# Optimization experiments

Measured on AMD Instinct MI355X. Metric: run time of the kernel, lower is better.

Reference implementation:

```python
import jax, jax.numpy as jnp
import numpy as np

D_MODEL = 2048; D_STATE = 128; D_CONV = 4; EXPAND = 2
HEADDIM = 64; NGROUPS = 1; CHUNK = 256
D_INNER = EXPAND * D_MODEL          # 4096
NHEADS = D_INNER // HEADDIM         # 64
HG = NHEADS // NGROUPS              # heads per group
CONV_DIM = D_INNER + 2 * NGROUPS * D_STATE          # 4352
D_IN_PROJ = 2 * D_INNER + 2 * NGROUPS * D_STATE + NHEADS  # 8512
BATCH = 2; SEQLEN = 2048
EPS = 1e-5


def setup_inputs() -> dict:
    ks = jax.random.split(jax.random.key(0), 8)
    u = jax.random.normal(ks[0], (BATCH, SEQLEN, D_MODEL), jnp.float32)
    in_proj_w = jax.random.normal(ks[1], (D_IN_PROJ, D_MODEL), jnp.float32) * D_MODEL ** -0.5
    conv_w = jax.random.normal(ks[2], (CONV_DIM, D_CONV), jnp.float32) * D_CONV ** -0.5
    conv_b = jax.random.normal(ks[3], (CONV_DIM,), jnp.float32) * 0.1
    # dt_bias init exactly as in the module: inv softplus of dt ~ U(log(1e-3), log(1e-1))
    dt = jnp.exp(jax.random.uniform(ks[4], (NHEADS,), jnp.float32)
                 * (np.float32(np.log(0.1)) - np.float32(np.log(0.001))) + np.float32(np.log(0.001)))
    dt = jnp.clip(dt, 1e-4, None)
    dt_bias = dt + jnp.log(-jnp.expm1(-dt))
    A_log = jnp.log(jax.random.uniform(ks[5], (NHEADS,), jnp.float32, minval=1.0, maxval=16.0))
    D_skip = jnp.ones((NHEADS,), jnp.float32)
    norm_w = jnp.ones((D_INNER,), jnp.float32)
    out_proj_w = jax.random.normal(ks[6], (D_MODEL, D_INNER), jnp.float32) * D_INNER ** -0.5
    return dict(u=u, in_proj_w=in_proj_w, conv_w=conv_w, conv_b=conv_b,
                dt_bias=dt_bias, A_log=A_log, D_skip=D_skip,
                norm_w=norm_w, out_proj_w=out_proj_w)


def _mamba2(u, in_proj_w, conv_w, conv_b, dt_bias, A_log, D_skip, norm_w, out_proj_w):
    b, l, _ = u.shape
    nc = l // CHUNK
    zxbcdt = u @ in_proj_w.T                                   # (b,l,d_in_proj)
    z = zxbcdt[..., :D_INNER]                                  # gate
    xBC = zxbcdt[..., D_INNER:D_INNER + CONV_DIM]
    dt = jax.nn.softplus(zxbcdt[..., D_INNER + CONV_DIM:] + dt_bias)  # (b,l,h)
    # causal depthwise conv1d (padding d_conv-1, truncated to seqlen) + SiLU
    xp = jnp.pad(xBC, ((0, 0), (D_CONV - 1, 0), (0, 0)))
    conv = conv_b + sum(conv_w[:, k] * xp[:, k:k + l, :] for k in range(D_CONV))
    xBC = jax.nn.silu(conv)
    x = xBC[..., :D_INNER].reshape(b, l, NHEADS, HEADDIM)
    Bm = xBC[..., D_INNER:D_INNER + NGROUPS * D_STATE].reshape(b, l, NGROUPS, D_STATE)
    Cm = xBC[..., D_INNER + NGROUPS * D_STATE:].reshape(b, l, NGROUPS, D_STATE)
    A = -jnp.exp(A_log)                                        # (h,)
    # ---- SSD chunked scan ----
    xc = x.reshape(b, nc, CHUNK, NGROUPS, HG, HEADDIM)         # (b,c,s,g,H,p)
    dtc = dt.reshape(b, nc, CHUNK, NGROUPS, HG)                # (b,c,s,g,H)
    Bc = Bm.reshape(b, nc, CHUNK, NGROUPS, D_STATE)            # (b,c,s,g,n)
    Cc = Cm.reshape(b, nc, CHUNK, NGROUPS, D_STATE)
    dA = jnp.transpose(dtc * A.reshape(NGROUPS, HG), (0, 3, 4, 1, 2))  # (b,g,H,c,s)
    dA_cs = jnp.cumsum(dA, axis=-1)                            # (b,g,H,c,s)
    # intra-chunk: L[i,j] = exp(sum_{j<k<=i} dA_k), lower-triangular (diag=1)
    seg = dA_cs[..., :, None] - dA_cs[..., None, :]            # (b,g,H,c,l,s)
    tri = jnp.tril(jnp.ones((CHUNK, CHUNK), bool))
    Lmat = jnp.where(tri, jnp.exp(seg), 0.0)
    xdt = xc * dtc[..., None]                                  # (b,c,s,g,H,p)
    CB = jnp.einsum('bclgn,bcsgn->bcgls', Cc, Bc)
    Y_diag = jnp.einsum('bcgls,bgHcls,bcsgHp->bclgHp', CB, Lmat, xdt)
    # chunk states and inter-chunk recurrence
    decay_states = jnp.exp(dA_cs[..., -1:] - dA_cs)            # (b,g,H,c,s)
    states = jnp.einsum('bcsgn,bgHcs,bcsgHp->bcgHpn', Bc, decay_states, xdt)
    chunk_decay = jnp.exp(dA_cs[..., -1])                      # (b,g,H,c)

    def step(carry, inp):
        st, dec = inp
        return carry * dec[..., None, None] + st, carry

    _, prev = jax.lax.scan(step, jnp.zeros_like(states[:, 0]),
                           (jnp.moveaxis(states, 1, 0), jnp.moveaxis(chunk_decay, -1, 0)))
    prev = jnp.moveaxis(prev, 0, 1)                            # (b,c,g,H,p,n) state entering chunk
    Y_off = jnp.einsum('bclgn,bcgHpn,bgHcl->bclgHp', Cc, prev, jnp.exp(dA_cs))
    y = (Y_diag + Y_off).reshape(b, l, NHEADS, HEADDIM) + x * D_skip[None, None, :, None]
    y = y.reshape(b, l, D_INNER)
    # gated RMSNorm: gate first (norm_before_gate=False), groupwise rms (ngroups=1 -> full)
    y = y * jax.nn.silu(z)
    yg = y.reshape(b, l, NGROUPS, D_INNER // NGROUPS)
    yg = yg * jax.lax.rsqrt(jnp.mean(yg * yg, axis=-1, keepdims=True) + EPS)
    y = yg.reshape(b, l, D_INNER) * norm_w
    return y @ out_proj_w.T                                    # (b,l,d_model)


def reference(u, in_proj_w, conv_w, conv_b, dt_bias, A_log, D_skip, norm_w, out_proj_w):
    return _mamba2(u, in_proj_w, conv_w, conv_b, dt_bias, A_log, D_skip, norm_w, out_proj_w)
```

## Files before the change

### kernel.cpp

```cpp
#include <hip/hip_runtime.h>
#include <hip/hip_bf16.h>


#define D_MODEL   2048
#define D_STATE   128
#define HEADDIM   64
#define CHUNK     256
#define D_INNER   4096
#define NHEADS    64
#define CONV_DIM  4352
#define D_IN_PROJ 8512
#define SEQLEN    2048
#define NC        8
#define ROWSTOT   4096
#define NPAD      8576
#define RMS_EPS   1e-5f

#define OFF_WIN   0ull
#define OFF_XBF   0ull
#define OFF_PREV  0ull
#define OFF_WOUT  16777216ull
#define OFF_UBF   35127296ull
#define OFF_DTV   35127296ull
#define OFF_DACS  36175872ull
#define OFF_BBF   37224448ull
#define OFF_CBF   38273024ull
#define OFF_CB    39321600ull
#define OFF_BT    43515904ull
#define OFF_XBC   51904512ull
#define OFF_STATE 51904512ull
#define OFF_ZBF   87556096ull
#define OFF_DTRAW 121110528ull
#define OFF_YBUF  121110528ull
#define WS_NEEDED 154664960ull

#define N4_U    2097152l
#define N4_WIN  4390912l

typedef __hip_bfloat16 bf16;
typedef __bf16 bfrag8 __attribute__((ext_vector_type(8)));
typedef float  f32x4v __attribute__((ext_vector_type(4)));

__device__ __forceinline__ f32x4v mfma16(bfrag8 a, bfrag8 b, f32x4v c) {
  return __builtin_amdgcn_mfma_f32_16x16x32_bf16(a, b, c, 0, 0, 0);
}

__device__ __forceinline__ void gload_lds16(const void* g, void* l) {
  __builtin_amdgcn_global_load_lds((const __attribute__((address_space(1))) void*)g,
                                   (__attribute__((address_space(3))) void*)l, 16, 0, 0);
}

__device__ __forceinline__ bf16 f2b(float x) { return __float2bfloat16(x); }
__device__ __forceinline__ float b2f(bf16 x) { return __bfloat162float(x); }
__device__ __forceinline__ float siluf(float x) { return x / (1.f + __expf(-x)); }

#define BARRIER() asm volatile("s_barrier" ::: "memory")
#define WAITV(N) asm volatile("s_waitcnt vmcnt(" #N ")" ::: "memory")
#define LGKM0()  asm volatile("s_waitcnt lgkmcnt(0)" ::: "memory")

__device__ __forceinline__ bfrag8 ds_read_b128f(const bf16* p) {
  bfrag8 d;
  unsigned a = (unsigned)(unsigned long long)p;
  asm volatile("ds_read_b128 %0, %1" : "=&v"(d) : "v"(a));
  return d;
}

__global__ __launch_bounds__(256) void cast_all_kernel(const float* __restrict__ u,
    const float* __restrict__ w_in,
    bf16* __restrict__ u_bf, bf16* __restrict__ win_bf) {
  long i = (long)blockIdx.x * 256 + threadIdx.x;
  if (i < N4_U) {
    float4 v = ((const float4*)u)[i];
    bf16* o = u_bf + i * 4;
    o[0] = f2b(v.x); o[1] = f2b(v.y); o[2] = f2b(v.z); o[3] = f2b(v.w);
  } else if (i < N4_U + N4_WIN) {
    long e = (i - N4_U) * 4;
    long row = e / D_MODEL;
    bf16* o = win_bf + e;
    if (row < D_IN_PROJ) {
      float4 v = *(const float4*)(w_in + e);
      o[0] = f2b(v.x); o[1] = f2b(v.y); o[2] = f2b(v.z); o[3] = f2b(v.w);
    } else {
      bf16 z = f2b(0.f);
      o[0] = z; o[1] = z; o[2] = z; o[3] = z;
    }
  }
}


__global__ __launch_bounds__(512) void gemm1_kernel(const bf16* __restrict__ A,
                                                    const bf16* __restrict__ B,
                                                    bf16* __restrict__ zb,
                                                    bf16* __restrict__ xbc,
                                                    float* __restrict__ dtraw) {
  int pid = blockIdx.x;
  int t = pid & 63, s = pid >> 6;
  int sm = s / 9, sn = s % 9;
  int xcd = t & 7, j8 = t >> 3;
  int tm = sm * 8 + (xcd >> 1) * 2 + (j8 & 1);
  int tn = sn * 8 + (xcd & 1) * 4 + (j8 >> 1);
  if (tn >= 67) return;
  long row0 = (long)tm * 256, col0 = (long)tn * 128;

  __shared__ __align__(16) bf16 As[2 * 256 * 32];
  __shared__ __align__(16) bf16 Bs[2 * 128 * 32];
  int tid = threadIdx.x, lane = tid & 63, w = tid >> 6;
  int wr = w >> 1, wc = w & 1, r16 = lane & 15, q = lane >> 4;
  int qs = (q ^ ((r16 >> 1) & 3)) * 8;
  const int K = D_MODEL;
  f32x4v zero4 = {0.f, 0.f, 0.f, 0.f};
  f32x4v acc[4][4];
#pragma unroll
  for (int i = 0; i < 4; ++i)
#pragma unroll
    for (int j = 0; j < 4; ++j) acc[i][j] = zero4;

  for (int kt = 0; kt < K; kt += 64) {
    __syncthreads();
#pragma unroll
    for (int j = 0; j < 4; ++j) {
      int ci = j * 512 + tid;
      int half = ci >> 10, cj = ci & 1023;
      int r = cj >> 2;
      int ko = half * 32 + ((cj & 3) ^ ((cj >> 3) & 3)) * 8;
      gload_lds16(A + (row0 + r) * (long)K + kt + ko,
                  (char*)As + j * 8192 + w * 1024);
    }
#pragma unroll
    for (int j = 0; j < 2; ++j) {
      int ci = j * 512 + tid;
      int half = ci >> 9, cj = ci & 511;
      int r = cj >> 2;
      int ko = half * 32 + ((cj & 3) ^ ((cj >> 3) & 3)) * 8;
      gload_lds16(B + (col0 + r) * (long)K + kt + ko,
                  (char*)Bs + j * 8192 + w * 1024);
    }
    __syncthreads();
#pragma unroll
    for (int ks = 0; ks < 2; ++ks) {
      const bf16* Ab = As + ks * 8192;
      const bf16* Bb = Bs + ks * 4096;
      bfrag8 af[4], bfv[4];
#pragma unroll
      for (int i = 0; i < 4; ++i) af[i]  = *(const bfrag8*)(Ab + (wr * 64 + i * 16 + r16) * 32 + qs);
#pragma unroll
      for (int i = 0; i < 4; ++i) bfv[i] = *(const bfrag8*)(Bb + (wc * 64 + i * 16 + r16) * 32 + qs);
#pragma unroll
      for (int i = 0; i < 4; ++i)
#pragma unroll
        for (int j = 0; j < 4; ++j) acc[i][j] = mfma16(af[i], bfv[j], acc[i][j]);
    }
  }
#pragma unroll
  for (int i = 0; i < 4; ++i)
#pragma unroll
    for (int j = 0; j < 4; ++j) {
      long col = col0 + wc * 64 + j * 16 + r16;
#pragma unroll
      for (int r = 0; r < 4; ++r) {
        long row = row0 + wr * 64 + i * 16 + q * 4 + r;
        float v = acc[i][j][r];
        if (col < D_INNER)                       zb[row * D_INNER + col] = f2b(v);
        else if (col < D_INNER + CONV_DIM)       xbc[row * CONV_DIM + (col - D_INNER)] = f2b(v);
        else if (col < D_IN_PROJ)                dtraw[row * NHEADS + (col - D_INNER - CONV_DIM)] = v;
      }
    }
}

template<int LD>
__device__ __forceinline__ void stage_half2(const bf16* __restrict__ src,
    long rowbeg, int kt, char* lds_slot, int tid, int w) {
  int r = tid >> 2;
  int ko0 = ((tid & 3) ^ ((tid >> 3) & 3)) * 8;
  const bf16* g0 = src + (rowbeg + r) * (long)LD + kt + ko0;
  gload_lds16(g0,      lds_slot + w * 1024);
  gload_lds16(g0 + 32, lds_slot + 8192 + w * 1024);
}

__global__ __launch_bounds__(512, 2) void gemm2_kernel(const bf16* __restrict__ A,
                                                       const bf16* __restrict__ Bw,
                                                       float* __restrict__ C) {
  int pid = blockIdx.x;
  int tn = (pid & 7) * 2 + (pid >> 7);
  int tm = (pid >> 3) & 15;
  long row0 = (long)tm * 256, col0 = (long)tn * 128;

  __shared__ __align__(16) bf16 As[6 * 8192];
  __shared__ __align__(16) bf16 Bs[3 * 8192];
  char* AsB = (char*)&As[0];
  char* BsB = (char*)&Bs[0];

  int tid = threadIdx.x, lane = tid & 63, w = tid >> 6;
  int r16 = lane & 15, qh = lane >> 4;
  int qs = (qh ^ ((r16 >> 1) & 3)) * 8;
  int wm = w >> 1, wn = w & 1;
  int hsel = wm >> 1;
  int rih = (wm & 1) * 64 + r16;
  int cb = wn * 64 + r16;

  f32x4v zero4 = {0.f, 0.f, 0.f, 0.f};
  f32x4v acc[4][4];
#pragma unroll
  for (int i = 0; i < 4; ++i)
#pragma unroll
    for (int j = 0; j < 4; ++j) acc[i][j] = zero4;

  stage_half2<D_INNER>(A,  row0,       0,  AsB + 0 * 16384, tid, w);
  stage_half2<D_INNER>(Bw, col0,       0,  BsB + 0 * 16384, tid, w);
  stage_half2<D_INNER>(A,  row0 + 128, 0,  AsB + 1 * 16384, tid, w);
  stage_half2<D_INNER>(A,  row0,       64, AsB + 2 * 16384, tid, w);
  stage_half2<D_INNER>(Bw, col0,       64, BsB + 1 * 16384, tid, w);
  stage_half2<D_INNER>(A,  row0 + 128, 64, AsB + 3 * 16384, tid, w);
  WAITV(6);
  BARRIER();

  int cur = 0, pf = 2;
#pragma unroll 1
  for (int tt = 0; tt < 64; ++tt) {
    int kpref = (tt < 62 ? tt + 2 : 63) * 64;
    const bf16* Asl = As + (cur * 2 + hsel) * 8192;
    const bf16* Bsl = Bs + cur * 8192;
    bfrag8 af[4], bfv[4];

#pragma unroll
    for (int i = 0; i < 4; ++i) af[i]  = ds_read_b128f(Asl + (rih + i * 16) * 32 + qs);
#pragma unroll
    for (int j = 0; j < 4; ++j) bfv[j] = ds_read_b128f(Bsl + (cb + j * 16) * 32 + qs);
    stage_half2<D_INNER>(A,  row0,       kpref, AsB + (pf * 2) * 16384, tid, w);
    stage_half2<D_INNER>(Bw, col0,       kpref, BsB + pf * 16384, tid, w);
    BARRIER();
    LGKM0();
    __builtin_amdgcn_sched_barrier(0);
    __builtin_amdgcn_s_setprio(1);
#pragma unroll
    for (int i = 0; i < 4; ++i)
#pragma unroll
      for (int j = 0; j < 4; ++j) acc[i][j] = mfma16(af[i], bfv[j], acc[i][j]);
    __builtin_amdgcn_s_setprio(0);
    BARRIER();

#pragma unroll
    for (int i = 0; i < 4; ++i) af[i]  = ds_read_b128f(Asl + 4096 + (rih + i * 16) * 32 + qs);
#pragma unroll
    for (int j = 0; j < 4; ++j) bfv[j] = ds_read_b128f(Bsl + 4096 + (cb + j * 16) * 32 + qs);
    stage_half2<D_INNER>(A,  row0 + 128, kpref, AsB + (pf * 2 + 1) * 16384, tid, w);
    WAITV(6);
    BARRIER();
    LGKM0();
    __builtin_amdgcn_sched_barrier(0);
    __builtin_amdgcn_s_setprio(1);
#pragma unroll
    for (int i = 0; i < 4; ++i)
#pragma unroll
      for (int j = 0; j < 4; ++j) acc[i][j] = mfma16(af[i], bfv[j], acc[i][j]);
    __builtin_amdgcn_s_setprio(0);
    BARRIER();

    cur = (cur == 2) ? 0 : cur + 1;
    pf  = (pf  == 2) ? 0 : pf + 1;
  }
  WAITV(0);

#pragma unroll
  for (int i = 0; i < 4; ++i)
#pragma unroll
    for (int j = 0; j < 4; ++j)
#pragma unroll
      for (int r = 0; r < 4; ++r) {
        long row = row0 + wm * 64 + i * 16 + qh * 4 + r;
        long col = col0 + wn * 64 + j * 16 + r16;
        C[row * (long)D_MODEL + col] = acc[i][j][r];
      }
}

__global__ __launch_bounds__(256) void conv_dt_kernel(
    const float* __restrict__ dtraw, const float* __restrict__ dt_bias,
    const float* __restrict__ A_log, float* __restrict__ dtv_buf,
    float* __restrict__ dacs_buf,
    const bf16* __restrict__ xbc, const float* __restrict__ conv_w,
    const float* __restrict__ conv_b, bf16* __restrict__ xo,
    bf16* __restrict__ Bo, bf16* __restrict__ Co, bf16* __restrict__ BT) {
  if (blockIdx.x < 1024) {
    int blk = blockIdx.x;
    int c = blk & 7, h = (blk >> 3) & 63, b = blk >> 9;
    int s = threadIdx.x, lane = s & 63, w = s >> 6;
    long row = (long)b * SEQLEN + c * CHUNK + s;
    float raw = dtraw[row * NHEADS + h] + dt_bias[h];
    float dtv = fmaxf(raw, 0.f) + log1pf(__expf(-fabsf(raw)));
    float A = -__expf(A_log[h]);
    float x = dtv * A;
#pragma unroll
    for (int off = 1; off < 64; off <<= 1) {
      float y = __shfl_up(x, off);
      if (lane >= off) x += y;
    }
    __shared__ __align__(16) float wsum[4];
    if (lane == 63) wsum[w] = x;
    __syncthreads();
    float pre = 0.f;
#pragma unroll
    for (int i = 0; i < 4; ++i) pre += (i < w) ? wsum[i] : 0.f;
    long o = ((long)(b * NHEADS + h) * NC + c) * CHUNK + s;
    dtv_buf[o] = dtv;
    dacs_buf[o] = x + pre;
    return;
  }
  int t = blockIdx.x - 1024;
  int bx = t % 17;
  int rest = t / 17;
  int by = rest & 255, bz = rest >> 8;
  int cidx = bx * 256 + threadIdx.x;
  int l0 = by * 8, b = bz;
  float4 wv = *(const float4*)(conv_w + cidx * 4);
  float bias = conv_b[cidx];
  const bf16* base = xbc + (long)b * SEQLEN * CONV_DIM + cidx;
  float win[11];
#pragma unroll
  for (int k = 0; k < 11; ++k) {
    int ls = l0 - 3 + k;
    win[k] = (ls >= 0) ? b2f(base[(long)ls * CONV_DIM]) : 0.f;
  }
  int cgrp = (cidx < D_INNER) ? 0 : ((cidx < D_INNER + D_STATE) ? 1 : 2);
  int n = cidx - D_INNER;
  int n2 = cidx - D_INNER - D_STATE;
  int cch = l0 >> 8;
#pragma unroll
  for (int j = 0; j < 8; ++j) {
    float acc = bias + wv.x * win[j] + wv.y * win[j + 1] + wv.z * win[j + 2] + wv.w * win[j + 3];
    bf16 o = f2b(siluf(acc));
    int l = l0 + j;
    long rowo = (long)b * SEQLEN + l;
    if (cgrp == 0) {
      xo[rowo * D_INNER + cidx] = o;
    } else if (cgrp == 1) {
      Bo[rowo * D_STATE + n] = o;
      BT[(((long)b * NC + cch) * D_STATE + n) * CHUNK + (l & 255)] = o;
    } else {
      Co[rowo * D_STATE + n2] = o;
    }
  }
}

__global__ __launch_bounds__(256) void cb_kernel(const bf16* __restrict__ Cg,
                                                 const bf16* __restrict__ Bg,
                                                 float* __restrict__ CB) {
  int blk = blockIdx.x;
  int stile = blk & 3, bc = blk >> 2;
  int c = bc & 7, b = bc >> 3;
  int tid = threadIdx.x, lane = tid & 63, w = tid >> 6, r16 = lane & 15, q = lane >> 4;
  const bf16* Cb = Cg + ((long)b * SEQLEN + c * CHUNK) * D_STATE;
  const bf16* Bb = Bg + ((long)b * SEQLEN + c * CHUNK) * D_STATE;
  bfrag8 af[4][4];
#pragma unroll
  for (int lt = 0; lt < 4; ++lt)
#pragma unroll
    for (int kk = 0; kk < 4; ++kk)
      af[lt][kk] = *(const bfrag8*)(Cb + (long)(w * 64 + lt * 16 + r16) * D_STATE + kk * 32 + q * 8);
  float* CBb = CB + (long)bc * CHUNK * CHUNK;
  f32x4v zero4 = {0.f, 0.f, 0.f, 0.f};
  for (int st = stile * 4; st < stile * 4 + 4; ++st) {
    f32x4v acc[4] = {zero4, zero4, zero4, zero4};
#pragma unroll
    for (int kk = 0; kk < 4; ++kk) {
      bfrag8 bfv = *(const bfrag8*)(Bb + (long)(st * 16 + r16) * D_STATE + kk * 32 + q * 8);
#pragma unroll
      for (int lt = 0; lt < 4; ++lt) acc[lt] = mfma16(af[lt][kk], bfv, acc[lt]);
    }
#pragma unroll
    for (int lt = 0; lt < 4; ++lt)
#pragma unroll
      for (int r = 0; r < 4; ++r)
        CBb[(long)(w * 64 + lt * 16 + q * 4 + r) * CHUNK + st * 16 + r16] = acc[lt][r];
  }
}

__global__ __launch_bounds__(256) void ssm_diag_kernel(
    const bf16* __restrict__ xg, const bf16* __restrict__ BT,
    const float* __restrict__ CB, const float* __restrict__ dtv_buf,
    const float* __restrict__ dacs_buf, const float* __restrict__ Dskip,
    bf16* __restrict__ ybuf, float* __restrict__ states) {
  int blk = blockIdx.x;
  int h = blk & 63, cc = (blk >> 6) & 7, b = blk >> 9;
  int tid = threadIdx.x, lane = tid & 63, w = tid >> 6, r16 = lane & 15, q = lane >> 4;

  __shared__ __align__(16) __bf16 xT[HEADDIM][264];
  __shared__ __align__(16) float cs_s[CHUNK];
  __shared__ __align__(16) float dt_s[CHUNK];
  __shared__ __align__(16) float w_s[CHUNK];

  long hco = ((long)(b * NHEADS + h) * NC + cc) * CHUNK;
  cs_s[tid] = dacs_buf[hco + tid];
  dt_s[tid] = dtv_buf[hco + tid];
  __syncthreads();
  float cl_last = cs_s[CHUNK - 1];
  w_s[tid] = __expf(cl_last - cs_s[tid]) * dt_s[tid];

  const __bf16* xbase = (const __bf16*)(xg + ((long)b * SEQLEN + cc * CHUNK) * D_INNER + h * HEADDIM);
#pragma unroll
  for (int it = 0; it < 8; ++it) {
    int e = it * 256 + tid;
    int s = e >> 3, p0 = (e & 7) * 8;
    bfrag8 xv = *(const bfrag8*)(xbase + (long)s * D_INNER + p0);
#pragma unroll
    for (int j = 0; j < 8; ++j) xT[p0 + j][s] = xv[j];
  }
  __syncthreads();

  const float* CBchunk = CB + (long)(b * NC + cc) * CHUNK * CHUNK;
  const __bf16* BTc = (const __bf16*)(BT + (((long)b * NC + cc) * D_STATE) * CHUNK);
  f32x4v zero4 = {0.f, 0.f, 0.f, 0.f};
  f32x4v accY[4][4], accS[2][4];
#pragma unroll
  for (int i = 0; i < 4; ++i)
#pragma unroll
    for (int j = 0; j < 4; ++j) accY[i][j] = zero4;
#pragma unroll
  for (int i = 0; i < 2; ++i)
#pragma unroll
    for (int j = 0; j < 4; ++j) accS[i][j] = zero4;

  int l_row[4];
  const float* CBrow[4];
#pragma unroll
  for (int lt = 0; lt < 4; ++lt) {
    l_row[lt] = w * 64 + lt * 16 + r16;
    CBrow[lt] = CBchunk + (long)l_row[lt] * CHUNK;
  }

#pragma unroll 2
  for (int ks = 0; ks < 8; ++ks) {
    int s0 = ks * 32 + q * 8;
    float4 cs0 = *(const float4*)(cs_s + s0);
    float4 cs1 = *(const float4*)(cs_s + s0 + 4);
    float4 dt0 = *(const float4*)(dt_s + s0);
    float4 dt1 = *(const float4*)(dt_s + s0 + 4);
    float4 w0  = *(const float4*)(w_s + s0);
    float4 w1  = *(const float4*)(w_s + s0 + 4);
    float csv[8] = {cs0.x, cs0.y, cs0.z, cs0.w, cs1.x, cs1.y, cs1.z, cs1.w};
    float dtv8[8] = {dt0.x, dt0.y, dt0.z, dt0.w, dt1.x, dt1.y, dt1.z, dt1.w};
    float wv8[8]  = {w0.x, w0.y, w0.z, w0.w, w1.x, w1.y, w1.z, w1.w};

    bfrag8 xf[4];
#pragma unroll
    for (int pt = 0; pt < 4; ++pt) xf[pt] = *(const bfrag8*)(&xT[pt * 16 + r16][s0]);

#pragma unroll
    for (int lt = 0; lt < 4; ++lt) {
      int l = l_row[lt];
      float cs_l = cs_s[l];
      float4 cb0 = *(const float4*)(CBrow[lt] + s0);
      float4 cb1 = *(const float4*)(CBrow[lt] + s0 + 4);
      float cbv[8] = {cb0.x, cb0.y, cb0.z, cb0.w, cb1.x, cb1.y, cb1.z, cb1.w};
      bfrag8 pf;
#pragma unroll
      for (int j = 0; j < 8; ++j) {
        float v = (s0 + j <= l)
                    ? cbv[j] * __expf(fminf(cs_l - csv[j], 0.f)) * dtv8[j]
                    : 0.f;
        pf[j] = (__bf16)v;
      }
#pragma unroll
      for (int pt = 0; pt < 4; ++pt) accY[lt][pt] = mfma16(pf, xf[pt], accY[lt][pt]);
    }

#pragma unroll
    for (int nt = 0; nt < 2; ++nt) {
      int n = w * 32 + nt * 16 + r16;
      bfrag8 braw = *(const bfrag8*)(BTc + (long)n * CHUNK + s0);
      bfrag8 bwf;
#pragma unroll
      for (int j = 0; j < 8; ++j) bwf[j] = (__bf16)((float)braw[j] * wv8[j]);
#pragma unroll
      for (int pt = 0; pt < 4; ++pt) accS[nt][pt] = mfma16(bwf, xf[pt], accS[nt][pt]);
    }
  }

  float dsk = Dskip[h];
  bf16* ybase = ybuf + ((long)b * SEQLEN + cc * CHUNK) * D_INNER + h * HEADDIM;
#pragma unroll
  for (int lt = 0; lt < 4; ++lt)
#pragma unroll
    for (int pt = 0; pt < 4; ++pt)
#pragma unroll
      for (int r = 0; r < 4; ++r) {
        int lrow = w * 64 + lt * 16 + q * 4 + r;
        int pcol = pt * 16 + r16;
        ybase[(long)lrow * D_INNER + pcol] = f2b(accY[lt][pt][r] + (float)xT[pcol][lrow] * dsk);
      }
  float* sbase = states + (long)blk * (HEADDIM * D_STATE);
#pragma unroll
  for (int nt = 0; nt < 2; ++nt)
#pragma unroll
    for (int pt = 0; pt < 4; ++pt)
#pragma unroll
      for (int r = 0; r < 4; ++r)
        sbase[(long)(pt * 16 + r16) * D_STATE + w * 32 + nt * 16 + q * 4 + r] = accS[nt][pt][r];
}

__global__ __launch_bounds__(256) void state_scan_kernel(const float* __restrict__ states,
    const float* __restrict__ dacs, bf16* __restrict__ prevb) {
  int gid = blockIdx.x;
  int et = gid & 31, bh = gid >> 5;
  int h = bh & 63, b = bh >> 6;
  int e = et * 256 + threadIdx.x;
  float dec[NC];
#pragma unroll
  for (int c = 0; c < NC; ++c)
    dec[c] = __expf(dacs[((long)(b * NHEADS + h) * NC + c) * CHUNK + (CHUNK - 1)]);
  float carry = 0.f;
#pragma unroll
  for (int c = 0; c < NC; ++c) {
    long off = ((long)((b * NC + c) * NHEADS + h)) * (HEADDIM * D_STATE) + e;
    prevb[off] = f2b(carry);
    carry = carry * dec[c] + states[off];
  }
}

__global__ __launch_bounds__(256) void yoff_kernel(const bf16* __restrict__ Cg,
    const bf16* __restrict__ prevb, const float* __restrict__ dacs,
    bf16* __restrict__ ybuf) {
  int blk = blockIdx.x;
  int h = blk & 63, cc = (blk >> 6) & 7, b = blk >> 9;
  int tid = threadIdx.x, lane = tid & 63, w = tid >> 6, r16 = lane & 15, q = lane >> 4;
  __shared__ __align__(16) float cs_s[CHUNK];
  cs_s[tid] = dacs[((long)(b * NHEADS + h) * NC + cc) * CHUNK + tid];
  __syncthreads();
  const bf16* Cb = Cg + ((long)b * SEQLEN + cc * CHUNK) * D_STATE;
  const bf16* Pb = prevb + (long)blk * (HEADDIM * D_STATE);
  f32x4v zero4 = {0.f, 0.f, 0.f, 0.f};
  f32x4v acc[4][4];
#pragma unroll
  for (int i = 0; i < 4; ++i)
#pragma unroll
    for (int j = 0; j < 4; ++j) acc[i][j] = zero4;
#pragma unroll
  for (int kk = 0; kk < 4; ++kk) {
    bfrag8 bv[4];
#pragma unroll
    for (int pt = 0; pt < 4; ++pt)
      bv[pt] = *(const bfrag8*)(Pb + (long)(pt * 16 + r16) * D_STATE + kk * 32 + q * 8);
#pragma unroll
    for (int lt = 0; lt < 4; ++lt) {
      bfrag8 av = *(const bfrag8*)(Cb + (long)(w * 64 + lt * 16 + r16) * D_STATE + kk * 32 + q * 8);
#pragma unroll
      for (int pt = 0; pt < 4; ++pt) acc[lt][pt] = mfma16(av, bv[pt], acc[lt][pt]);
    }
  }
  bf16* ybase = ybuf + ((long)b * SEQLEN + cc * CHUNK) * D_INNER + h * HEADDIM;
#pragma unroll
  for (int lt = 0; lt < 4; ++lt)
#pragma unroll
    for (int pt = 0; pt < 4; ++pt)
#pragma unroll
      for (int r = 0; r < 4; ++r) {
        int lrow = w * 64 + lt * 16 + q * 4 + r;
        float ef = __expf(cs_s[lrow]);
        bf16* p = ybase + (long)lrow * D_INNER + pt * 16 + r16;
        *p = f2b(b2f(*p) + acc[lt][pt][r] * ef);
      }
}

__global__ __launch_bounds__(256) void cast_gate_kernel(
    const float* __restrict__ w_out, bf16* __restrict__ wout_bf,
    bf16* __restrict__ ybuf, const bf16* __restrict__ zb,
    const float* __restrict__ norm_w) {
  if (blockIdx.x < 8192) {
    long i = (long)blockIdx.x * 256 + threadIdx.x;
    float4 v = ((const float4*)w_out)[i];
    bf16* o = wout_bf + i * 4;
    o[0] = f2b(v.x); o[1] = f2b(v.y); o[2] = f2b(v.z); o[3] = f2b(v.w);
    return;
  }
  int row = blockIdx.x - 8192, tid = threadIdx.x;
  bf16* y = ybuf + (long)row * D_INNER;
  const bf16* z = zb + (long)row * D_INNER;
  float v[16];
  float ss = 0.f;
#pragma unroll
  for (int i = 0; i < 2; ++i) {
    int e = tid * 16 + i * 8;
    bfrag8 yv = *(const bfrag8*)(y + e);
    bfrag8 zv = *(const bfrag8*)(z + e);
#pragma unroll
    for (int j = 0; j < 8; ++j) {
      float a = (float)yv[j] * siluf((float)zv[j]);
      v[i * 8 + j] = a;
      ss += a * a;
    }
  }
#pragma unroll
  for (int off = 32; off > 0; off >>= 1) ss += __shfl_down(ss, off);
  __shared__ __align__(16) float red[4];
  int lane = tid & 63, w = tid >> 6;
  if (lane == 0) red[w] = ss;
  __syncthreads();
  float tot = red[0] + red[1] + red[2] + red[3];
  float scale = rsqrtf(tot * (1.f / D_INNER) + RMS_EPS);
#pragma unroll
  for (int i = 0; i < 2; ++i) {
    int e = tid * 16 + i * 8;
    float4 w0 = *(const float4*)(norm_w + e);
    float4 w1 = *(const float4*)(norm_w + e + 4);
    bfrag8 o;
    o[0] = (__bf16)(v[i * 8 + 0] * scale * w0.x);
    o[1] = (__bf16)(v[i * 8 + 1] * scale * w0.y);
    o[2] = (__bf16)(v[i * 8 + 2] * scale * w0.z);
    o[3] = (__bf16)(v[i * 8 + 3] * scale * w0.w);
    o[4] = (__bf16)(v[i * 8 + 4] * scale * w1.x);
    o[5] = (__bf16)(v[i * 8 + 5] * scale * w1.y);
    o[6] = (__bf16)(v[i * 8 + 6] * scale * w1.z);
    o[7] = (__bf16)(v[i * 8 + 7] * scale * w1.w);
    *(bfrag8*)(y + e) = o;
  }
}

extern "C" void kernel_launch(void* const* d_in, const int* in_sizes, int n_in,
                              void* d_out, int out_size, void* d_ws, size_t ws_size,
                              hipStream_t stream) {
  if (ws_size < WS_NEEDED) return;

  const float* u       = (const float*)d_in[0];
  const float* w_in    = (const float*)d_in[1];
  const float* conv_w  = (const float*)d_in[2];
  const float* conv_b  = (const float*)d_in[3];
  const float* dt_bias = (const float*)d_in[4];
  const float* A_log   = (const float*)d_in[5];
  const float* Dskip   = (const float*)d_in[6];
  const float* norm_w  = (const float*)d_in[7];
  const float* w_out   = (const float*)d_in[8];
  float* out = (float*)d_out;

  char* ws = (char*)d_ws;
  bf16*  win_bf  = (bf16*)(ws + OFF_WIN);
  bf16*  x_bf    = (bf16*)(ws + OFF_XBF);
  bf16*  prevb   = (bf16*)(ws + OFF_PREV);
  bf16*  wout_bf = (bf16*)(ws + OFF_WOUT);
  bf16*  u_bf    = (bf16*)(ws + OFF_UBF);
  float* dtv     = (float*)(ws + OFF_DTV);
  float* dacs    = (float*)(ws + OFF_DACS);
  bf16*  B_bf    = (bf16*)(ws + OFF_BBF);
  bf16*  C_bf    = (bf16*)(ws + OFF_CBF);
  float* CBb     = (float*)(ws + OFF_CB);
  bf16*  BT_bf   = (bf16*)(ws + OFF_BT);
  bf16*  xbc_bf  = (bf16*)(ws + OFF_XBC);
  float* states  = (float*)(ws + OFF_STATE);
  bf16*  z_bf    = (bf16*)(ws + OFF_ZBF);
  float* dt_raw  = (float*)(ws + OFF_DTRAW);
  bf16*  ybuf    = (bf16*)(ws + OFF_YBUF);

  cast_all_kernel<<<25344, 256, 0, stream>>>(u, w_in, u_bf, win_bf);
  gemm1_kernel<<<1152, 512, 0, stream>>>(u_bf, win_bf, z_bf, xbc_bf, dt_raw);
  conv_dt_kernel<<<9728, 256, 0, stream>>>(dt_raw, dt_bias, A_log, dtv, dacs,
                                           xbc_bf, conv_w, conv_b, x_bf, B_bf, C_bf, BT_bf);
  cb_kernel<<<64, 256, 0, stream>>>(C_bf, B_bf, CBb);
  ssm_diag_kernel<<<1024, 256, 0, stream>>>(x_bf, BT_bf, CBb, dtv, dacs, Dskip, ybuf, states);
  state_scan_kernel<<<4096, 256, 0, stream>>>(states, dacs, prevb);
  yoff_kernel<<<1024, 256, 0, stream>>>(C_bf, prevb, dacs, ybuf);
  cast_gate_kernel<<<12288, 256, 0, stream>>>(w_out, wout_bf, ybuf, z_bf, norm_w);
  gemm2_kernel<<<256, 512, 0, stream>>>(ybuf, wout_bf, out);
}
```

Before: 551.9 us.

## Rewrite in-projection GEMM with triple-buffered LDS prefetch pipeline and XCD-aware tile mapping

Replaces the simple load-sync-compute in-projection GEMM with the pipelined structure already used by the out-projection GEMM. It uses three LDS stages with two K-tiles of prefetch in flight, waits on vmcnt, and raises wave priority around the MFMA bursts. The grid shrinks from 1152 to 1072 blocks, with a new XCD-interleaved tile mapping that launches only valid tiles. The aim is to hide global-to-LDS load latency behind MFMA work, at the cost of more LDS per block and a two-blocks-per-CU occupancy constraint.

Result: slower. 568.3 us (+3.0%).

```diff
diff --git a/kernel.cpp b/kernel.cpp
--- a/kernel.cpp
+++ b/kernel.cpp
@@ -88,85 +88,6 @@
 }
 
 
-__global__ __launch_bounds__(512) void gemm1_kernel(const bf16* __restrict__ A,
-                                                    const bf16* __restrict__ B,
-                                                    bf16* __restrict__ zb,
-                                                    bf16* __restrict__ xbc,
-                                                    float* __restrict__ dtraw) {
-  int pid = blockIdx.x;
-  int t = pid & 63, s = pid >> 6;
-  int sm = s / 9, sn = s % 9;
-  int xcd = t & 7, j8 = t >> 3;
-  int tm = sm * 8 + (xcd >> 1) * 2 + (j8 & 1);
-  int tn = sn * 8 + (xcd & 1) * 4 + (j8 >> 1);
-  if (tn >= 67) return;
-  long row0 = (long)tm * 256, col0 = (long)tn * 128;
-
-  __shared__ __align__(16) bf16 As[2 * 256 * 32];
-  __shared__ __align__(16) bf16 Bs[2 * 128 * 32];
-  int tid = threadIdx.x, lane = tid & 63, w = tid >> 6;
-  int wr = w >> 1, wc = w & 1, r16 = lane & 15, q = lane >> 4;
-  int qs = (q ^ ((r16 >> 1) & 3)) * 8;
-  const int K = D_MODEL;
-  f32x4v zero4 = {0.f, 0.f, 0.f, 0.f};
-  f32x4v acc[4][4];
-#pragma unroll
-  for (int i = 0; i < 4; ++i)
-#pragma unroll
-    for (int j = 0; j < 4; ++j) acc[i][j] = zero4;
-
-  for (int kt = 0; kt < K; kt += 64) {
-    __syncthreads();
-#pragma unroll
-    for (int j = 0; j < 4; ++j) {
-      int ci = j * 512 + tid;
-      int half = ci >> 10, cj = ci & 1023;
-      int r = cj >> 2;
-      int ko = half * 32 + ((cj & 3) ^ ((cj >> 3) & 3)) * 8;
-      gload_lds16(A + (row0 + r) * (long)K + kt + ko,
-                  (char*)As + j * 8192 + w * 1024);
-    }
-#pragma unroll
-    for (int j = 0; j < 2; ++j) {
-      int ci = j * 512 + tid;
-      int half = ci >> 9, cj = ci & 511;
-      int r = cj >> 2;
-      int ko = half * 32 + ((cj & 3) ^ ((cj >> 3) & 3)) * 8;
-      gload_lds16(B + (col0 + r) * (long)K + kt + ko,
-                  (char*)Bs + j * 8192 + w * 1024);
-    }
-    __syncthreads();
-#pragma unroll
-    for (int ks = 0; ks < 2; ++ks) {
-      const bf16* Ab = As + ks * 8192;
-      const bf16* Bb = Bs + ks * 4096;
-      bfrag8 af[4], bfv[4];
-#pragma unroll
-      for (int i = 0; i < 4; ++i) af[i]  = *(const bfrag8*)(Ab + (wr * 64 + i * 16 + r16) * 32 + qs);
-#pragma unroll
-      for (int i = 0; i < 4; ++i) bfv[i] = *(const bfrag8*)(Bb + (wc * 64 + i * 16 + r16) * 32 + qs);
-#pragma unroll
-      for (int i = 0; i < 4; ++i)
-#pragma unroll
-        for (int j = 0; j < 4; ++j) acc[i][j] = mfma16(af[i], bfv[j], acc[i][j]);
-    }
-  }
-#pragma unroll
-  for (int i = 0; i < 4; ++i)
-#pragma unroll
-    for (int j = 0; j < 4; ++j) {
-      long col = col0 + wc * 64 + j * 16 + r16;
-#pragma unroll
-      for (int r = 0; r < 4; ++r) {
-        long row = row0 + wr * 64 + i * 16 + q * 4 + r;
-        float v = acc[i][j][r];
-        if (col < D_INNER)                       zb[row * D_INNER + col] = f2b(v);
-        else if (col < D_INNER + CONV_DIM)       xbc[row * CONV_DIM + (col - D_INNER)] = f2b(v);
-        else if (col < D_IN_PROJ)                dtraw[row * NHEADS + (col - D_INNER - CONV_DIM)] = v;
-      }
-    }
-}
-
 template<int LD>
 __device__ __forceinline__ void stage_half2(const bf16* __restrict__ src,
     long rowbeg, int kt, char* lds_slot, int tid, int w) {
@@ -175,6 +96,109 @@
   const bf16* g0 = src + (rowbeg + r) * (long)LD + kt + ko0;
   gload_lds16(g0,      lds_slot + w * 1024);
   gload_lds16(g0 + 32, lds_slot + 8192 + w * 1024);
+}
+
+__global__ __launch_bounds__(512, 2) void gemm1_kernel(const bf16* __restrict__ A,
+                                                       const bf16* __restrict__ Bw,
+                                                       bf16* __restrict__ zb,
+                                                       bf16* __restrict__ xbc,
+                                                       float* __restrict__ dtraw) {
+  int pid = blockIdx.x;
+  int wgid = (pid & 7) * 134 + (pid >> 3);
+  int tn = wgid >> 4;
+  int tm = wgid & 15;
+  long row0 = (long)tm * 256, col0 = (long)tn * 128;
+
+  __shared__ __align__(16) bf16 As[6 * 8192];
+  __shared__ __align__(16) bf16 Bs[3 * 8192];
+  char* AsB = (char*)&As[0];
+  char* BsB = (char*)&Bs[0];
+
+  int tid = threadIdx.x, lane = tid & 63, w = tid >> 6;
+  int r16 = lane & 15, qh = lane >> 4;
+  int qs = (qh ^ ((r16 >> 1) & 3)) * 8;
+  int wm = w >> 1, wn = w & 1;
+  int hsel = wm >> 1;
+  int rih = (wm & 1) * 64 + r16;
+  int cb = wn * 64 + r16;
+
+  f32x4v zero4 = {0.f, 0.f, 0.f, 0.f};
+  f32x4v acc[4][4];
+#pragma unroll
+  for (int i = 0; i < 4; ++i)
+#pragma unroll
+    for (int j = 0; j < 4; ++j) acc[i][j] = zero4;
+
+  stage_half2<D_MODEL>(A,  row0,       0,  AsB + 0 * 16384, tid, w);
+  stage_half2<D_MODEL>(Bw, col0,       0,  BsB + 0 * 16384, tid, w);
+  stage_half2<D_MODEL>(A,  row0 + 128, 0,  AsB + 1 * 16384, tid, w);
+  stage_half2<D_MODEL>(A,  row0,       64, AsB + 2 * 16384, tid, w);
+  stage_half2<D_MODEL>(Bw, col0,       64, BsB + 1 * 16384, tid, w);
+  stage_half2<D_MODEL>(A,  row0 + 128, 64, AsB + 3 * 16384, tid, w);
+  WAITV(6);
+  BARRIER();
+
+  int cur = 0, pf = 2;
+#pragma unroll 1
+  for (int tt = 0; tt < 32; ++tt) {
+    int kpref = (tt < 30 ? tt + 2 : 31) * 64;
+    const bf16* Asl = As + (cur * 2 + hsel) * 8192;
+    const bf16* Bsl = Bs + cur * 8192;
+    bfrag8 af[4], bfv[4];
+
+#pragma unroll
+    for (int i = 0; i < 4; ++i) af[i]  = ds_read_b128f(Asl + (rih + i * 16) * 32 + qs);
+#pragma unroll
+    for (int j = 0; j < 4; ++j) bfv[j] = ds_read_b128f(Bsl + (cb + j * 16) * 32 + qs);
+    stage_half2<D_MODEL>(A,  row0,       kpref, AsB + (pf * 2) * 16384, tid, w);
+    stage_half2<D_MODEL>(Bw, col0,       kpref, BsB + pf * 16384, tid, w);
+    BARRIER();
+    LGKM0();
+    __builtin_amdgcn_sched_barrier(0);
+    __builtin_amdgcn_s_setprio(1);
+#pragma unroll
+    for (int i = 0; i < 4; ++i)
+#pragma unroll
+      for (int j = 0; j < 4; ++j) acc[i][j] = mfma16(af[i], bfv[j], acc[i][j]);
+    __builtin_amdgcn_s_setprio(0);
+    BARRIER();
+
+#pragma unroll
+    for (int i = 0; i < 4; ++i) af[i]  = ds_read_b128f(Asl + 4096 + (rih + i * 16) * 32 + qs);
+#pragma unroll
+    for (int j = 0; j < 4; ++j) bfv[j] = ds_read_b128f(Bsl + 4096 + (cb + j * 16) * 32 + qs);
+    stage_half2<D_MODEL>(A,  row0 + 128, kpref, AsB + (pf * 2 + 1) * 16384, tid, w);
+    WAITV(6);
+    BARRIER();
+    LGKM0();
+    __builtin_amdgcn_sched_barrier(0);
+    __builtin_amdgcn_s_setprio(1);
+#pragma unroll
+    for (int i = 0; i < 4; ++i)
+#pragma unroll
+      for (int j = 0; j < 4; ++j) acc[i][j] = mfma16(af[i], bfv[j], acc[i][j]);
+    __builtin_amdgcn_s_setprio(0);
+    BARRIER();
+
+    cur = (cur == 2) ? 0 : cur + 1;
+    pf  = (pf  == 2) ? 0 : pf + 1;
+  }
+  WAITV(0);
+
+#pragma unroll
+  for (int i = 0; i < 4; ++i)
+#pragma unroll
+    for (int j = 0; j < 4; ++j) {
+      long col = col0 + wn * 64 + j * 16 + r16;
+#pragma unroll
+      for (int r = 0; r < 4; ++r) {
+        long row = row0 + wm * 64 + i * 16 + qh * 4 + r;
+        float v = acc[i][j][r];
+        if (col < D_INNER)                       zb[row * D_INNER + col] = f2b(v);
+        else if (col < D_INNER + CONV_DIM)       xbc[row * CONV_DIM + (col - D_INNER)] = f2b(v);
+        else if (col < D_IN_PROJ)                dtraw[row * NHEADS + (col - D_INNER - CONV_DIM)] = v;
+      }
+    }
 }
 
 __global__ __launch_bounds__(512, 2) void gemm2_kernel(const bf16* __restrict__ A,
@@ -649,7 +673,7 @@
   bf16*  ybuf    = (bf16*)(ws + OFF_YBUF);
 
   cast_all_kernel<<<25344, 256, 0, stream>>>(u, w_in, u_bf, win_bf);
-  gemm1_kernel<<<1152, 512, 0, stream>>>(u_bf, win_bf, z_bf, xbc_bf, dt_raw);
+  gemm1_kernel<<<1072, 512, 0, stream>>>(u_bf, win_bf, z_bf, xbc_bf, dt_raw);
   conv_dt_kernel<<<9728, 256, 0, stream>>>(dt_raw, dt_bias, A_log, dtv, dacs,
                                            xbc_bf, conv_w, conv_b, x_bf, B_bf, C_bf, BT_bf);
   cb_kernel<<<64, 256, 0, stream>>>(C_bf, B_bf, CBb);
```

## Store conv x output pre-transposed per chunk and DMA it swizzled into LDS

Applied to the files above, without the earlier changes.

The conv kernel now writes the x channels in a chunk-blocked layout: eight consecutive sequence positions per channel are packed into one 16-byte vector store, replacing scattered 2-byte stores. The SSM diagonal kernel then loads x straight into shared memory with global-to-LDS 16-byte loads, using an XOR swizzle to spread LDS banks, instead of doing an element-by-element transpose scatter into a padded shared array. The aim is to cut uncoalesced global writes and LDS transpose work. The cost is that this x layout is specific to these two kernels, and any other consumer of x must match it.

After: 554.4 us. About the same (+0.4%).

```diff
diff --git a/kernel.cpp b/kernel.cpp
--- a/kernel.cpp
+++ b/kernel.cpp
@@ -320,19 +320,30 @@
     int ls = l0 - 3 + k;
     win[k] = (ls >= 0) ? b2f(base[(long)ls * CONV_DIM]) : 0.f;
   }
-  int cgrp = (cidx < D_INNER) ? 0 : ((cidx < D_INNER + D_STATE) ? 1 : 2);
+  int cch = l0 >> 8;
+  if (cidx < D_INNER) {
+    int sc = (l0 & 255) >> 3;
+    bfrag8 o8;
+#pragma unroll
+    for (int j = 0; j < 8; ++j) {
+      float acc = bias + wv.x * win[j] + wv.y * win[j + 1] + wv.z * win[j + 2] + wv.w * win[j + 3];
+      bf16 tb = f2b(siluf(acc));
+      o8[j] = *reinterpret_cast<__bf16*>(&tb);
+    }
+    long off = (((long)(b * NC + cch) * 32 + sc) << 15) + ((long)cidx << 3);
+    *(bfrag8*)(xo + off) = o8;
+    return;
+  }
+  int cgrp = (cidx < D_INNER + D_STATE) ? 1 : 2;
   int n = cidx - D_INNER;
   int n2 = cidx - D_INNER - D_STATE;
-  int cch = l0 >> 8;
 #pragma unroll
   for (int j = 0; j < 8; ++j) {
     float acc = bias + wv.x * win[j] + wv.y * win[j + 1] + wv.z * win[j + 2] + wv.w * win[j + 3];
     bf16 o = f2b(siluf(acc));
     int l = l0 + j;
     long rowo = (long)b * SEQLEN + l;
-    if (cgrp == 0) {
-      xo[rowo * D_INNER + cidx] = o;
-    } else if (cgrp == 1) {
+    if (cgrp == 1) {
       Bo[rowo * D_STATE + n] = o;
       BT[(((long)b * NC + cch) * D_STATE + n) * CHUNK + (l & 255)] = o;
     } else {
@@ -383,7 +394,7 @@
   int h = blk & 63, cc = (blk >> 6) & 7, b = blk >> 9;
   int tid = threadIdx.x, lane = tid & 63, w = tid >> 6, r16 = lane & 15, q = lane >> 4;
 
-  __shared__ __align__(16) __bf16 xT[HEADDIM][264];
+  __shared__ __align__(16) __bf16 xT2[16384];
   __shared__ __align__(16) float cs_s[CHUNK];
   __shared__ __align__(16) float dt_s[CHUNK];
   __shared__ __align__(16) float w_s[CHUNK];
@@ -391,23 +402,24 @@
   long hco = ((long)(b * NHEADS + h) * NC + cc) * CHUNK;
   cs_s[tid] = dacs_buf[hco + tid];
   dt_s[tid] = dtv_buf[hco + tid];
+
+  long ccb = (long)(b * NC + cc) * 32;
+#pragma unroll
+  for (int it = 0; it < 8; ++it) {
+    int e = it * 256 + tid;
+    int p = e >> 5;
+    int sc = (e & 31) ^ (p & 7);
+    const bf16* src = xg + (((ccb + sc) * NHEADS + h) << 9) + (p << 3);
+    gload_lds16(src, (char*)xT2 + (it * 256 + (tid & ~63)) * 16);
+  }
   __syncthreads();
   float cl_last = cs_s[CHUNK - 1];
   w_s[tid] = __expf(cl_last - cs_s[tid]) * dt_s[tid];
-
-  const __bf16* xbase = (const __bf16*)(xg + ((long)b * SEQLEN + cc * CHUNK) * D_INNER + h * HEADDIM);
-#pragma unroll
-  for (int it = 0; it < 8; ++it) {
-    int e = it * 256 + tid;
-    int s = e >> 3, p0 = (e & 7) * 8;
-    bfrag8 xv = *(const bfrag8*)(xbase + (long)s * D_INNER + p0);
-#pragma unroll
-    for (int j = 0; j < 8; ++j) xT[p0 + j][s] = xv[j];
-  }
   __syncthreads();
 
   const float* CBchunk = CB + (long)(b * NC + cc) * CHUNK * CHUNK;
   const __bf16* BTc = (const __bf16*)(BT + (((long)b * NC + cc) * D_STATE) * CHUNK);
+  const char* xTb = (const char*)xT2;
   f32x4v zero4 = {0.f, 0.f, 0.f, 0.f};
   f32x4v accY[4][4], accS[2][4];
 #pragma unroll
@@ -442,7 +454,10 @@
 
     bfrag8 xf[4];
 #pragma unroll
-    for (int pt = 0; pt < 4; ++pt) xf[pt] = *(const bfrag8*)(&xT[pt * 16 + r16][s0]);
+    for (int pt = 0; pt < 4; ++pt) {
+      int p = pt * 16 + r16;
+      xf[pt] = *(const bfrag8*)(xTb + p * 512 + ((((ks << 2) + q) ^ (p & 7)) << 4));
+    }
 
 #pragma unroll
     for (int lt = 0; lt < 4; ++lt) {
@@ -485,7 +500,9 @@
       for (int r = 0; r < 4; ++r) {
         int lrow = w * 64 + lt * 16 + q * 4 + r;
         int pcol = pt * 16 + r16;
-        ybase[(long)lrow * D_INNER + pcol] = f2b(accY[lt][pt][r] + (float)xT[pcol][lrow] * dsk);
+        float xs = (float)*(const __bf16*)(xTb + pcol * 512 +
+                     ((((lrow >> 3) ^ (pcol & 7)) << 4)) + ((lrow & 7) << 1));
+        ybase[(long)lrow * D_INNER + pcol] = f2b(accY[lt][pt][r] + xs * dsk);
       }
   float* sbase = states + (long)blk * (HEADDIM * D_STATE);
 #pragma unroll
```

## Triple-buffer gemm1 K-loop with async LDS prefetch two stages ahead

Applied to the files above, without the earlier changes.

Replaces the synchronous double-barrier K loop (64-wide steps) in the input-projection GEMM with a 3-slot LDS ring of 32-wide K steps. Global-to-LDS loads are issued two iterations ahead and gated by vmcnt waits, so there is one barrier per iteration, and MFMA issue is given raised wave priority. This aims to hide global load latency behind compute. In exchange it doubles the iteration count, adds launch_bounds occupancy hints, and issues a redundant tail prefetch.

Measured after the change: 548.9 us. About the same (-0.6%).

```diff
diff --git a/kernel.cpp b/kernel.cpp
--- a/kernel.cpp
+++ b/kernel.cpp
@@ -88,11 +88,21 @@
 }
 
 
-__global__ __launch_bounds__(512) void gemm1_kernel(const bf16* __restrict__ A,
-                                                    const bf16* __restrict__ B,
-                                                    bf16* __restrict__ zb,
-                                                    bf16* __restrict__ xbc,
-                                                    float* __restrict__ dtraw) {
+__device__ __forceinline__ void stage_g1(const bf16* __restrict__ A,
+    const bf16* __restrict__ B, long row0, long col0, int kt,
+    char* slot, int tid, int w) {
+  int r = tid >> 2;
+  int ko = ((tid & 3) ^ ((tid >> 3) & 3)) * 8;
+  gload_lds16(A + (row0 + r) * (long)D_MODEL + kt + ko,       slot + w * 1024);
+  gload_lds16(A + (row0 + 128 + r) * (long)D_MODEL + kt + ko, slot + 8192 + w * 1024);
+  gload_lds16(B + (col0 + r) * (long)D_MODEL + kt + ko,       slot + 16384 + w * 1024);
+}
+
+__global__ __launch_bounds__(512, 4) void gemm1_kernel(const bf16* __restrict__ A,
+                                                       const bf16* __restrict__ B,
+                                                       bf16* __restrict__ zb,
+                                                       bf16* __restrict__ xbc,
+                                                       float* __restrict__ dtraw) {
   int pid = blockIdx.x;
   int t = pid & 63, s = pid >> 6;
   int sm = s / 9, sn = s % 9;
@@ -102,12 +112,12 @@
   if (tn >= 67) return;
   long row0 = (long)tm * 256, col0 = (long)tn * 128;
 
-  __shared__ __align__(16) bf16 As[2 * 256 * 32];
-  __shared__ __align__(16) bf16 Bs[2 * 128 * 32];
+  __shared__ __align__(16) bf16 Gs[3 * 12288];
+  char* lds = (char*)&Gs[0];
+
   int tid = threadIdx.x, lane = tid & 63, w = tid >> 6;
   int wr = w >> 1, wc = w & 1, r16 = lane & 15, q = lane >> 4;
   int qs = (q ^ ((r16 >> 1) & 3)) * 8;
-  const int K = D_MODEL;
   f32x4v zero4 = {0.f, 0.f, 0.f, 0.f};
   f32x4v acc[4][4];
 #pragma unroll
@@ -115,42 +125,36 @@
 #pragma unroll
     for (int j = 0; j < 4; ++j) acc[i][j] = zero4;
 
-  for (int kt = 0; kt < K; kt += 64) {
-    __syncthreads();
-#pragma unroll
-    for (int j = 0; j < 4; ++j) {
-      int ci = j * 512 + tid;
-      int half = ci >> 10, cj = ci & 1023;
-      int r = cj >> 2;
-      int ko = half * 32 + ((cj & 3) ^ ((cj >> 3) & 3)) * 8;
-      gload_lds16(A + (row0 + r) * (long)K + kt + ko,
-                  (char*)As + j * 8192 + w * 1024);
-    }
-#pragma unroll
-    for (int j = 0; j < 2; ++j) {
-      int ci = j * 512 + tid;
-      int half = ci >> 9, cj = ci & 511;
-      int r = cj >> 2;
-      int ko = half * 32 + ((cj & 3) ^ ((cj >> 3) & 3)) * 8;
-      gload_lds16(B + (col0 + r) * (long)K + kt + ko,
-                  (char*)Bs + j * 8192 + w * 1024);
-    }
-    __syncthreads();
-#pragma unroll
-    for (int ks = 0; ks < 2; ++ks) {
-      const bf16* Ab = As + ks * 8192;
-      const bf16* Bb = Bs + ks * 4096;
-      bfrag8 af[4], bfv[4];
-#pragma unroll
-      for (int i = 0; i < 4; ++i) af[i]  = *(const bfrag8*)(Ab + (wr * 64 + i * 16 + r16) * 32 + qs);
-#pragma unroll
-      for (int i = 0; i < 4; ++i) bfv[i] = *(const bfrag8*)(Bb + (wc * 64 + i * 16 + r16) * 32 + qs);
-#pragma unroll
-      for (int i = 0; i < 4; ++i)
-#pragma unroll
-        for (int j = 0; j < 4; ++j) acc[i][j] = mfma16(af[i], bfv[j], acc[i][j]);
-    }
-  }
+  stage_g1(A, B, row0, col0, 0,  lds + 0 * 24576, tid, w);
+  stage_g1(A, B, row0, col0, 32, lds + 1 * 24576, tid, w);
+
+  int cur = 0;
+#pragma unroll 1
+  for (int tt = 0; tt < 64; ++tt) {
+    const bf16* Asl = (const bf16*)(lds + cur * 24576);
+    const bf16* Bsl = Asl + 8192;
+    WAITV(3);
+    BARRIER();
+    bfrag8 af[4], bfv[4];
+#pragma unroll
+    for (int i = 0; i < 4; ++i) af[i]  = ds_read_b128f(Asl + (wr * 64 + i * 16 + r16) * 32 + qs);
+#pragma unroll
+    for (int j = 0; j < 4; ++j) bfv[j] = ds_read_b128f(Bsl + (wc * 64 + j * 16 + r16) * 32 + qs);
+    int pf = cur + 2; if (pf >= 3) pf -= 3;
+    int kpref = (tt + 2 < 64 ? tt + 2 : 63) * 32;
+    stage_g1(A, B, row0, col0, kpref, lds + pf * 24576, tid, w);
+    LGKM0();
+    __builtin_amdgcn_sched_barrier(0);
+    __builtin_amdgcn_s_setprio(1);
+#pragma unroll
+    for (int i = 0; i < 4; ++i)
+#pragma unroll
+      for (int j = 0; j < 4; ++j) acc[i][j] = mfma16(af[i], bfv[j], acc[i][j]);
+    __builtin_amdgcn_s_setprio(0);
+    cur = cur + 1; if (cur >= 3) cur -= 3;
+  }
+  WAITV(0);
+
 #pragma unroll
   for (int i = 0; i < 4; ++i)
 #pragma unroll
```
